# Performance work log

Hardware: AMD Instinct MI355X
Metric: run time of the kernel (lower is better)

The kernel has to match this reference:

```python
import jax, jax.numpy as jnp
import numpy as np

E, L, D, H, S, B = 8, 12, 768, 12, 512, 32
DIMS = [12, 8, 8, 8, 8, 12]
RANKS = [1, 8, 8, 8, 8, 8, 1]
ALPHA = 8.0


def setup_inputs() -> dict:
    key = jax.random.key(0)
    ks = iter(jax.random.split(key, 32))
    inp = {}
    inp['hidden_states'] = jax.random.normal(next(ks), (B, S, D), jnp.float32)
    inp['router_weights'] = jax.random.normal(next(ks), (D, E), jnp.float32)
    for pre in ('q', 'v'):
        for i in range(6):
            shp = (E, L, RANKS[i], DIMS[i], RANKS[i + 1])
            inp[f'{pre}_core{i}'] = jax.random.normal(next(ks), shp, jnp.float32) * 0.05
    for nm in ('Wq', 'Wk', 'Wv', 'Wo'):
        inp[nm] = jax.random.normal(next(ks), (L, D, D), jnp.float32) * 0.02
    for nm in ('bq', 'bk', 'bv', 'bo'):
        inp[nm] = jnp.zeros((L, D), jnp.float32)
    inp['ln_scale'] = jnp.ones((L, D), jnp.float32)
    inp['ln_bias'] = jnp.zeros((L, D), jnp.float32)
    return inp


def _layernorm(x, scale, bias, eps=1e-12):
    mu = x.mean(-1, keepdims=True)
    var = ((x - mu) ** 2).mean(-1, keepdims=True)
    return (x - mu) * jax.lax.rsqrt(var + eps) * scale + bias


def _tt_weights(cores):
    # cores[i]: [L, r_i, d_i, r_{i+1}]; chained TT contraction, vectorized over layers
    w = jnp.einsum('Lijk,Lklm,Lmno,Lopq,Lqrs,Lstu->Ljlnprt', *cores)
    return w.reshape(w.shape[0], D, D)  # [L, out, in] (matches torch weight.reshape)


def reference(hidden_states, router_weights,
              q_core0, q_core1, q_core2, q_core3, q_core4, q_core5,
              v_core0, v_core1, v_core2, v_core3, v_core4, v_core5,
              Wq, Wk, Wv, Wo, bq, bk, bv, bo, ln_scale, ln_bias):
    # routing: pool over sequence, softmax + argmax per sample
    pooled = hidden_states.mean(axis=1)                      # [B, D]
    probs = jax.nn.softmax(pooled @ router_weights, axis=-1)  # [B, E]
    idx = jnp.argmax(probs, axis=-1)                          # [B]
    e = idx[-1]
    qc = [c[e] for c in (q_core0, q_core1, q_core2, q_core3, q_core4, q_core5)]
    vc = [c[e] for c in (v_core0, v_core1, v_core2, v_core3, v_core4, v_core5)]
    Wq_a = Wq + ALPHA * _tt_weights(qc)  # [L, D, D]
    Wv_a = Wv + ALPHA * _tt_weights(vc)

    hd = D // H
    scale = 1.0 / jnp.sqrt(jnp.float32(hd))
    x = hidden_states
    for l in range(L):
        q = (x @ Wq_a[l].T + bq[l]).reshape(B, S, H, hd)
        k = (x @ Wk[l].T + bk[l]).reshape(B, S, H, hd)
        v = (x @ Wv_a[l].T + bv[l]).reshape(B, S, H, hd)
        scores = jnp.einsum('bqhd,bkhd->bhqk', q, k) * scale
        attn = jax.nn.softmax(scores, axis=-1)
        ctx = jnp.einsum('bhqk,bkhd->bqhd', attn, v).reshape(B, S, D)
        out = ctx @ Wo[l].T + bo[l]
        x = _layernorm(x + out, ln_scale[l], ln_bias[l])
    return x
```

## Files before the change

kernel.cpp:

```cpp
#include <hip/hip_runtime.h>
#include <hip/hip_bf16.h>
#include <stdint.h>

#define E_ 8
#define L_ 12
#define D_ 768
#define H_ 12
#define S_ 512
#define B_ 32
#define BS_ (B_*S_)

typedef __attribute__((ext_vector_type(4))) float floatx4;
typedef __attribute__((ext_vector_type(8))) __bf16 bf16x8;
typedef __attribute__((ext_vector_type(4))) __bf16 bf16x4;

__device__ __forceinline__ __bf16 f2bf(float f) {
  unsigned u = __builtin_bit_cast(unsigned, f);
  u += 0x7fffu + ((u >> 16) & 1u);
  unsigned short h = (unsigned short)(u >> 16);
  return __builtin_bit_cast(__bf16, h);
}

__device__ __forceinline__ float fexp2(float x) {
#if __has_builtin(__builtin_amdgcn_exp2f)
  return __builtin_amdgcn_exp2f(x);
#else
  return exp2f(x);
#endif
}

__device__ __forceinline__ void async16(const void* g, void* l) {
  __builtin_amdgcn_global_load_lds((__attribute__((address_space(1))) void*)g,
                                   (__attribute__((address_space(3))) void*)l,
                                   16, 0, 0);
}

__global__ void routing_pool_kernel(const float* __restrict__ hidden,
                                    float* __restrict__ partial) {
  const int blk = blockIdx.x;
  const int tid = threadIdx.x;
  const float* base = hidden + (size_t)(B_-1)*S_*D_ + (size_t)blk*8*D_;
  float acc[3] = {0.f, 0.f, 0.f};
  for (int s = 0; s < 8; ++s) {
#pragma unroll
    for (int i = 0; i < 3; ++i)
      acc[i] += base[(size_t)s*D_ + tid + i*256];
  }
#pragma unroll
  for (int i = 0; i < 3; ++i) partial[(size_t)blk*D_ + tid + i*256] = acc[i];
}

__global__ void routing_finish_kernel(const float* __restrict__ partial,
                                      const float* __restrict__ rw,
                                      int* __restrict__ e_out) {
  __shared__ float pooled[D_];
  __shared__ float logits[E_];
  int tid = threadIdx.x;
#pragma unroll
  for (int i = 0; i < 3; ++i) {
    int d = tid + i*256;
    float s = 0.f;
    for (int blk = 0; blk < 64; ++blk) s += partial[(size_t)blk*D_ + d];
    pooled[d] = s;
  }
  __syncthreads();
  if (tid < E_) {
    float s = 0.f;
    for (int d = 0; d < D_; ++d) s += pooled[d] * rw[d*E_ + tid];
    logits[tid] = s;
  }
  __syncthreads();
  if (tid == 0) {
    int best = 0; float bvv = logits[0];
    for (int e = 1; e < E_; ++e) if (logits[e] > bvv) { bvv = logits[e]; best = e; }
    e_out[0] = best;
  }
}

__global__ void convert_bf16_kernel(const float* __restrict__ src, __bf16* __restrict__ dst) {
  size_t i = ((size_t)blockIdx.x*256 + threadIdx.x)*8;
  __bf16 r[8];
#pragma unroll
  for (int j = 0; j < 8; ++j) r[j] = f2bf(src[i+j]);
  *(bf16x8*)(dst + i) = *(bf16x8*)r;
}

__global__ void convert_wk_kernel(const float* __restrict__ wk, __bf16* __restrict__ wqkv) {
  size_t i = ((size_t)blockIdx.x*256 + threadIdx.x)*8;
  int l = (int)(i / (D_*D_));
  int rem = (int)(i % (D_*D_));
  int n = rem / D_, k = rem % D_;
  __bf16 r[8];
#pragma unroll
  for (int j = 0; j < 8; ++j) r[j] = f2bf(wk[i+j]);
  *(bf16x8*)(wqkv + (size_t)l*2304*D_ + (size_t)(768+n)*D_ + k) = *(bf16x8*)r;
}

__global__ void tt_prep_kernel(
    const float* __restrict__ qc0, const float* __restrict__ qc1, const float* __restrict__ qc2,
    const float* __restrict__ qc3, const float* __restrict__ qc4, const float* __restrict__ qc5,
    const float* __restrict__ vc0, const float* __restrict__ vc1, const float* __restrict__ vc2,
    const float* __restrict__ vc3, const float* __restrict__ vc4, const float* __restrict__ vc5,
    const float* __restrict__ Wq, const float* __restrict__ Wv,
    const int* __restrict__ e_idx, __bf16* __restrict__ wqkv) {
  const int l = blockIdx.x;
  const int pre = blockIdx.y;
  const int z = blockIdx.z;
  const int tid = threadIdx.x;
  const int e = e_idx[0];
  const float* c0 = (pre ? vc0 : qc0) + (size_t)(e*L_ + l)*96;
  const float* c1 = (pre ? vc1 : qc1) + (size_t)(e*L_ + l)*512;
  const float* c2 = (pre ? vc2 : qc2) + (size_t)(e*L_ + l)*512;
  const float* c3 = (pre ? vc3 : qc3) + (size_t)(e*L_ + l)*512;
  const float* c4 = (pre ? vc4 : qc4) + (size_t)(e*L_ + l)*512;
  const float* c5 = (pre ? vc5 : qc5) + (size_t)(e*L_ + l)*96;
  __shared__ float M1[768];
  __shared__ float R2[768];
  __shared__ float M2[6144];
  __shared__ float Rm[6144];
  for (int idx = tid; idx < 768; idx += 256) {
    int j = idx >> 6, rem = idx & 63, l2 = rem >> 3, m = rem & 7;
    float s = 0.f;
    for (int k = 0; k < 8; ++k) s += c0[j*8 + k] * c1[k*64 + l2*8 + m];
    M1[idx] = s;
    int qq = idx / 96, rem2 = idx % 96, rr = rem2 / 12, t = rem2 % 12;
    float s2 = 0.f;
    for (int si = 0; si < 8; ++si) s2 += c4[qq*64 + rr*8 + si] * c5[si*12 + t];
    R2[idx] = s2;
  }
  __syncthreads();
  for (int idx = tid; idx < 6144; idx += 256) {
    int o = idx & 7, n = (idx >> 3) & 7, jl = idx >> 6;
    float s = 0.f;
    for (int m = 0; m < 8; ++m) s += M1[jl*8 + m] * c2[m*64 + n*8 + o];
    M2[idx] = s;
    int o2 = idx / 768, inp = idx % 768, p = inp / 96, rt = inp % 96;
    float s2 = 0.f;
    for (int qq = 0; qq < 8; ++qq) s2 += c3[o2*64 + p*8 + qq] * R2[qq*96 + rt];
    Rm[idx] = s2;
  }
  __syncthreads();
  const float* Wbase = (pre ? Wv : Wq) + (size_t)l*D_*D_;
  __bf16* dst = wqkv + (size_t)l*2304*D_ + (pre ? (size_t)1536*D_ : 0);
  for (int g = tid; g < 48*96; g += 256) {
    const int outr = z*48 + (g / 96);
    const int inp0 = (g % 96) * 8;
    float m2r[8];
#pragma unroll
    for (int o = 0; o < 8; ++o) m2r[o] = M2[outr*8 + o];
    float acc[8];
#pragma unroll
    for (int u = 0; u < 8; ++u) acc[u] = 0.f;
#pragma unroll
    for (int o = 0; o < 8; ++o) {
      float4 r0 = *(const float4*)&Rm[o*768 + inp0];
      float4 r1 = *(const float4*)&Rm[o*768 + inp0 + 4];
      acc[0] += m2r[o]*r0.x; acc[1] += m2r[o]*r0.y;
      acc[2] += m2r[o]*r0.z; acc[3] += m2r[o]*r0.w;
      acc[4] += m2r[o]*r1.x; acc[5] += m2r[o]*r1.y;
      acc[6] += m2r[o]*r1.z; acc[7] += m2r[o]*r1.w;
    }
    const float* wb = Wbase + (size_t)outr*768 + inp0;
    float4 w0 = *(const float4*)wb;
    float4 w1 = *(const float4*)(wb + 4);
    __bf16 r[8];
    r[0] = f2bf(w0.x + 8.f*acc[0]); r[1] = f2bf(w0.y + 8.f*acc[1]);
    r[2] = f2bf(w0.z + 8.f*acc[2]); r[3] = f2bf(w0.w + 8.f*acc[3]);
    r[4] = f2bf(w1.x + 8.f*acc[4]); r[5] = f2bf(w1.y + 8.f*acc[5]);
    r[6] = f2bf(w1.z + 8.f*acc[6]); r[7] = f2bf(w1.w + 8.f*acc[7]);
    *(bf16x8*)(dst + (size_t)outr*768 + inp0) = *(bf16x8*)r;
  }
}

#define SLOT_BYTES 28672
template<bool SPLITV>
__global__ __launch_bounds__(512, 2) void gemm_bt(
    const __bf16* __restrict__ A, const __bf16* __restrict__ Bw,
    const float* __restrict__ bq, const float* __restrict__ bk, const float* __restrict__ bvp,
    __bf16* __restrict__ outb, __bf16* __restrict__ vtout, int Nw) {
  __shared__ __align__(16) char lds[4*SLOT_BYTES];
  const int tid = threadIdx.x;
  const int w = tid >> 6, lane = tid & 63;
  const int quad = lane >> 4, l16 = lane & 15;
  const int wm = w >> 2, wn = w & 3;
  const size_t mblk = (size_t)blockIdx.y * 256;
  const size_t nblk = (size_t)blockIdx.x * 192;
  const __bf16* Ag = A + mblk * 768;
  const __bf16* Bg = Bw + nblk * 768;

  int a_goff[2], a_loff[2];
#pragma unroll
  for (int i = 0; i < 2; ++i) {
    int line = w*16 + i*8 + (lane >> 3);
    int s8 = (lane & 7) ^ (line & 7);
    int row = 2*line + (s8 >> 2);
    a_goff[i] = row*768 + (s8 & 3)*8;
    a_loff[i] = (w*16 + i*8)*128;
  }
  int b_goff[2], b_loff[2];
#pragma unroll
  for (int i = 0; i < 2; ++i) {
    int bl0 = (w < 4) ? (w*16 + i*8) : (64 + (w-4)*8);
    int line = bl0 + (lane >> 3);
    int s8 = (lane & 7) ^ (line & 7);
    int row = 2*line + (s8 >> 2);
    b_goff[i] = row*768 + (s8 & 3)*8;
    b_loff[i] = 16384 + bl0*128;
  }

  int a_foff[8], b_foff[3];
#pragma unroll
  for (int mf = 0; mf < 8; ++mf) {
    int r = wm*128 + mf*16 + l16;
    int line = r >> 1, s8 = (r & 1)*4 + quad, ph = s8 ^ (line & 7);
    a_foff[mf] = line*128 + ph*16;
  }
#pragma unroll
  for (int nf = 0; nf < 3; ++nf) {
    int r = wn*48 + nf*16 + l16;
    int line = r >> 1, s8 = (r & 1)*4 + quad, ph = s8 ^ (line & 7);
    b_foff[nf] = 16384 + line*128 + ph*16;
  }

  floatx4 acc[8][3];
#pragma unroll
  for (int mf = 0; mf < 8; ++mf)
#pragma unroll
    for (int nf = 0; nf < 3; ++nf) acc[mf][nf] = {0.f,0.f,0.f,0.f};

  auto STAGE = [&](int t) {
    const __bf16* Ab = Ag + t*32;
    const __bf16* Bb = Bg + t*32;
    char* ls = lds + (t & 3)*SLOT_BYTES;
    async16(Ab + a_goff[0], ls + a_loff[0]);
    async16(Ab + a_goff[1], ls + a_loff[1]);
    if (w < 4) {
      async16(Bb + b_goff[0], ls + b_loff[0]);
      async16(Bb + b_goff[1], ls + b_loff[1]);
    } else {
      async16(Bb + b_goff[0], ls + b_loff[0]);
    }
  };

  bf16x8 af[8], bfr[3];
  auto LOAD1 = [&](int u) {
    const char* ls = lds + (u & 3)*SLOT_BYTES;
#pragma unroll
    for (int nf = 0; nf < 3; ++nf) bfr[nf] = *(const bf16x8*)(ls + b_foff[nf]);
#pragma unroll
    for (int mf = 0; mf < 4; ++mf) af[mf] = *(const bf16x8*)(ls + a_foff[mf]);
  };
  auto LOAD2 = [&](int u) {
    const char* ls = lds + (u & 3)*SLOT_BYTES;
#pragma unroll
    for (int mf = 4; mf < 8; ++mf) af[mf] = *(const bf16x8*)(ls + a_foff[mf]);
  };
  auto MM = [&](int mf0) {
    __builtin_amdgcn_s_setprio(1);
#pragma unroll
    for (int mf = mf0; mf < mf0 + 4; ++mf)
#pragma unroll
      for (int nf = 0; nf < 3; ++nf)
        acc[mf][nf] = __builtin_amdgcn_mfma_f32_16x16x32_bf16(af[mf], bfr[nf], acc[mf][nf], 0, 0, 0);
    __builtin_amdgcn_s_setprio(0);
  };
  auto BAR = [&]() {
    __builtin_amdgcn_s_barrier();
    __builtin_amdgcn_sched_barrier(0);
  };

  STAGE(0); STAGE(1); STAGE(2);
  if (w < 4) asm volatile("s_waitcnt vmcnt(8)" ::: "memory");
  else       asm volatile("s_waitcnt vmcnt(6)" ::: "memory");
  BAR();

  for (int u = 0; u < 21; ++u) {
    LOAD1(u);
    BAR();
    MM(0);
    LOAD2(u);
    STAGE(u + 3);
    if (w < 4) asm volatile("s_waitcnt vmcnt(8)" ::: "memory");
    else       asm volatile("s_waitcnt vmcnt(6)" ::: "memory");
    BAR();
    MM(4);
  }
  LOAD1(21);
  BAR();
  MM(0);
  LOAD2(21);
  if (w < 4) asm volatile("s_waitcnt vmcnt(4)" ::: "memory");
  else       asm volatile("s_waitcnt vmcnt(3)" ::: "memory");
  BAR();
  MM(4);
  LOAD1(22);
  BAR();
  MM(0);
  LOAD2(22);
  asm volatile("s_waitcnt vmcnt(0)" ::: "memory");
  BAR();
  MM(4);
  LOAD1(23);
  BAR();
  MM(0);
  LOAD2(23);
  BAR();
  MM(4);

  if (SPLITV && blockIdx.x >= 8) {
#pragma unroll
    for (int nf = 0; nf < 3; ++nf) {
      const int vcol = (int)nblk - 1536 + wn*48 + nf*16 + l16;
      const int h = vcol >> 6, d = vcol & 63;
      const float bval = bvp[vcol];
#pragma unroll
      for (int mf = 0; mf < 8; ++mf) {
        const int mrow = (int)mblk + wm*128 + mf*16 + quad*4;
        const int b = mrow >> 9, s = mrow & 511;
        __bf16 pr[4];
#pragma unroll
        for (int r = 0; r < 4; ++r) pr[r] = f2bf(acc[mf][nf][r] + bval);
        *(bf16x4*)(vtout + (size_t)((b*H_ + h)*64 + d)*S_ + s) = *(bf16x4*)pr;
      }
    }
    return;
  }
  const float* bias = bq;
  if (SPLITV) bias = (blockIdx.x < 4) ? bq : bk;
  float bval[3]; int ncol[3];
#pragma unroll
  for (int nf = 0; nf < 3; ++nf) {
    ncol[nf] = (int)nblk + wn*48 + nf*16 + l16;
    int bc = ncol[nf]; if (bc >= 768) bc -= 768;
    bval[nf] = bias[bc];
  }
#pragma unroll
  for (int mf = 0; mf < 8; ++mf) {
#pragma unroll
    for (int nf = 0; nf < 3; ++nf) {
#pragma unroll
      for (int r = 0; r < 4; ++r) {
        const int mrow = (int)mblk + wm*128 + mf*16 + quad*4 + r;
        outb[(size_t)mrow*Nw + ncol[nf]] = f2bf(acc[mf][nf][r] + bval[nf]);
      }
    }
  }
}

#define PSTR 72
__global__ __launch_bounds__(256) void flash_kernel(const __bf16* __restrict__ qkv,
                                                    const __bf16* __restrict__ vt,
                                                    __bf16* __restrict__ ctx) {
  __shared__ __align__(16) __bf16 Qs[64*PSTR];
  __shared__ __align__(16) __bf16 Ks[64*PSTR];
  __shared__ __align__(16) __bf16 Vts[64*PSTR];
  __shared__ __align__(16) __bf16 Ps[64*PSTR];
  const int tid = threadIdx.x;
  const int w = tid >> 6, lane = tid & 63;
  const int quad = lane >> 4, l16 = lane & 15;
  const int n = blockIdx.x;
  const int bh = (n >> 6)*8 + (n & 7);
  const int q0 = ((n >> 3) & 7) * 64;
  const int b = bh / H_, h = bh % H_;
  const float SCL = 0.125f * 1.44269504f;

  {
#pragma unroll
    for (int it = 0; it < 2; ++it) {
      int slot = it*256 + tid, row = slot >> 3, seg = slot & 7;
      bf16x8 v = *(const bf16x8*)(qkv + (size_t)(b*S_ + q0 + row)*2304 + h*64 + seg*8);
      *(bf16x8*)&Qs[row*PSTR + seg*8] = v;
    }
  }

  floatx4 acc_o[4];
#pragma unroll
  for (int jd = 0; jd < 4; ++jd) acc_o[jd] = {0.f,0.f,0.f,0.f};
  float m_prev = -__builtin_inff();
  float l_part = 0.f;

  for (int kt = 0; kt < 8; ++kt) {
    __syncthreads();
#pragma unroll
    for (int it = 0; it < 2; ++it) {
      int slot = it*256 + tid, row = slot >> 3, seg = slot & 7;
      bf16x8 kvv = *(const bf16x8*)(qkv + (size_t)(b*S_ + kt*64 + row)*2304 + 768 + h*64 + seg*8);
      bf16x8 vtv = *(const bf16x8*)(vt + (size_t)(bh*64 + row)*S_ + kt*64 + seg*8);
      *(bf16x8*)&Ks[row*PSTR + seg*8] = kvv;
      *(bf16x8*)&Vts[row*PSTR + seg*8] = vtv;
    }
    __syncthreads();
    floatx4 sacc[4];
#pragma unroll
    for (int i = 0; i < 4; ++i) sacc[i] = {0.f,0.f,0.f,0.f};
#pragma unroll
    for (int kk = 0; kk < 64; kk += 32) {
      bf16x8 bq_ = *(const bf16x8*)&Qs[(w*16 + l16)*PSTR + kk + quad*8];
#pragma unroll
      for (int i = 0; i < 4; ++i) {
        bf16x8 ak = *(const bf16x8*)&Ks[(i*16 + l16)*PSTR + kk + quad*8];
        sacc[i] = __builtin_amdgcn_mfma_f32_16x16x32_bf16(ak, bq_, sacc[i], 0, 0, 0);
      }
    }
    float sv[4][4];
#pragma unroll
    for (int i = 0; i < 4; ++i)
#pragma unroll
      for (int r = 0; r < 4; ++r) sv[i][r] = sacc[i][r] * SCL;
    float mloc = sv[0][0];
#pragma unroll
    for (int i = 0; i < 4; ++i)
#pragma unroll
      for (int r = 0; r < 4; ++r) mloc = fmaxf(mloc, sv[i][r]);
    mloc = fmaxf(mloc, __shfl_xor(mloc, 16));
    mloc = fmaxf(mloc, __shfl_xor(mloc, 32));
    float mnew = fmaxf(m_prev, mloc);
    float alpha = fexp2(m_prev - mnew);
    m_prev = mnew;
    float rsum = 0.f;
#pragma unroll
    for (int i = 0; i < 4; ++i) {
      __bf16 pr[4];
#pragma unroll
      for (int r = 0; r < 4; ++r) {
        float p = fexp2(sv[i][r] - mnew);
        rsum += p;
        pr[r] = f2bf(p);
      }
      *(bf16x4*)&Ps[(w*16 + l16)*PSTR + i*16 + quad*4] = *(bf16x4*)pr;
    }
    l_part = l_part*alpha + rsum;
    float ab[4];
#pragma unroll
    for (int r = 0; r < 4; ++r) ab[r] = __shfl(alpha, quad*4 + r);
#pragma unroll
    for (int jd = 0; jd < 4; ++jd)
#pragma unroll
      for (int r = 0; r < 4; ++r) acc_o[jd][r] *= ab[r];
#pragma unroll
    for (int kk = 0; kk < 64; kk += 32) {
      bf16x8 ap = *(const bf16x8*)&Ps[(w*16 + l16)*PSTR + kk + quad*8];
#pragma unroll
      for (int jd = 0; jd < 4; ++jd) {
        bf16x8 bv_ = *(const bf16x8*)&Vts[(jd*16 + l16)*PSTR + kk + quad*8];
        acc_o[jd] = __builtin_amdgcn_mfma_f32_16x16x32_bf16(ap, bv_, acc_o[jd], 0, 0, 0);
      }
    }
  }
  float l_tot = l_part;
  l_tot += __shfl_xor(l_tot, 16);
  l_tot += __shfl_xor(l_tot, 32);
  float lb[4];
#pragma unroll
  for (int r = 0; r < 4; ++r) lb[r] = __shfl(l_tot, quad*4 + r);
#pragma unroll
  for (int jd = 0; jd < 4; ++jd) {
    const int d = jd*16 + l16;
#pragma unroll
    for (int r = 0; r < 4; ++r) {
      const int q = q0 + w*16 + quad*4 + r;
      ctx[(size_t)(b*S_ + q)*D_ + h*64 + d] = f2bf(acc_o[jd][r] / lb[r]);
    }
  }
}

template<bool FIRST, bool LAST>
__global__ __launch_bounds__(256) void ln_kernel(const float* __restrict__ residf,
                                                 __bf16* xb,
                                                 const __bf16* __restrict__ proj,
                                                 const float* __restrict__ gamma,
                                                 const float* __restrict__ beta,
                                                 float* __restrict__ xoutf) {
  const int tid = threadIdx.x;
  const int w = tid >> 6, lane = tid & 63;
  const int row = blockIdx.x*4 + w;
  const size_t base = (size_t)row * D_;
  const int c0 = lane*8;
  const bool has2 = lane < 32;
  const int c1 = 512 + lane*8;

  float v0[8], v1[8];
  {
    bf16x8 p0 = *(const bf16x8*)(proj + base + c0);
    if (FIRST) {
      float4 a = *(const float4*)(residf + base + c0);
      float4 bq4 = *(const float4*)(residf + base + c0 + 4);
      v0[0]=a.x+(float)p0[0]; v0[1]=a.y+(float)p0[1]; v0[2]=a.z+(float)p0[2]; v0[3]=a.w+(float)p0[3];
      v0[4]=bq4.x+(float)p0[4]; v0[5]=bq4.y+(float)p0[5]; v0[6]=bq4.z+(float)p0[6]; v0[7]=bq4.w+(float)p0[7];
    } else {
      bf16x8 r0 = *(const bf16x8*)(xb + base + c0);
#pragma unroll
      for (int j = 0; j < 8; ++j) v0[j] = (float)r0[j] + (float)p0[j];
    }
    if (has2) {
      bf16x8 p1 = *(const bf16x8*)(proj + base + c1);
      if (FIRST) {
        float4 a = *(const float4*)(residf + base + c1);
        float4 bq4 = *(const float4*)(residf + base + c1 + 4);
        v1[0]=a.x+(float)p1[0]; v1[1]=a.y+(float)p1[1]; v1[2]=a.z+(float)p1[2]; v1[3]=a.w+(float)p1[3];
        v1[4]=bq4.x+(float)p1[4]; v1[5]=bq4.y+(float)p1[5]; v1[6]=bq4.z+(float)p1[6]; v1[7]=bq4.w+(float)p1[7];
      } else {
        bf16x8 r1 = *(const bf16x8*)(xb + base + c1);
#pragma unroll
        for (int j = 0; j < 8; ++j) v1[j] = (float)r1[j] + (float)p1[j];
      }
    } else {
#pragma unroll
      for (int j = 0; j < 8; ++j) v1[j] = 0.f;
    }
  }
  float s = 0.f;
#pragma unroll
  for (int j = 0; j < 8; ++j) s += v0[j] + v1[j];
#pragma unroll
  for (int off = 32; off; off >>= 1) s += __shfl_xor(s, off);
  const float mu = s * (1.f/768.f);
  float q = 0.f;
#pragma unroll
  for (int j = 0; j < 8; ++j) { float d0 = v0[j]-mu; q += d0*d0; }
  if (has2) {
#pragma unroll
    for (int j = 0; j < 8; ++j) { float d1 = v1[j]-mu; q += d1*d1; }
  }
#pragma unroll
  for (int off = 32; off; off >>= 1) q += __shfl_xor(q, off);
  const float rs = rsqrtf(q * (1.f/768.f) + 1e-12f);

  {
    float4 g0 = *(const float4*)(gamma + c0);
    float4 g1 = *(const float4*)(gamma + c0 + 4);
    float4 b0 = *(const float4*)(beta + c0);
    float4 b1 = *(const float4*)(beta + c0 + 4);
    float o[8];
    o[0]=(v0[0]-mu)*rs*g0.x+b0.x; o[1]=(v0[1]-mu)*rs*g0.y+b0.y;
    o[2]=(v0[2]-mu)*rs*g0.z+b0.z; o[3]=(v0[3]-mu)*rs*g0.w+b0.w;
    o[4]=(v0[4]-mu)*rs*g1.x+b1.x; o[5]=(v0[5]-mu)*rs*g1.y+b1.y;
    o[6]=(v0[6]-mu)*rs*g1.z+b1.z; o[7]=(v0[7]-mu)*rs*g1.w+b1.w;
    if (LAST) {
      *(float4*)(xoutf + base + c0)     = {o[0],o[1],o[2],o[3]};
      *(float4*)(xoutf + base + c0 + 4) = {o[4],o[5],o[6],o[7]};
    } else {
      __bf16 ob[8];
#pragma unroll
      for (int j = 0; j < 8; ++j) ob[j] = f2bf(o[j]);
      *(bf16x8*)(xb + base + c0) = *(bf16x8*)ob;
    }
  }
  if (has2) {
    float4 g0 = *(const float4*)(gamma + c1);
    float4 g1 = *(const float4*)(gamma + c1 + 4);
    float4 b0 = *(const float4*)(beta + c1);
    float4 b1 = *(const float4*)(beta + c1 + 4);
    float o[8];
    o[0]=(v1[0]-mu)*rs*g0.x+b0.x; o[1]=(v1[1]-mu)*rs*g0.y+b0.y;
    o[2]=(v1[2]-mu)*rs*g0.z+b0.z; o[3]=(v1[3]-mu)*rs*g0.w+b0.w;
    o[4]=(v1[4]-mu)*rs*g1.x+b1.x; o[5]=(v1[5]-mu)*rs*g1.y+b1.y;
    o[6]=(v1[6]-mu)*rs*g1.z+b1.z; o[7]=(v1[7]-mu)*rs*g1.w+b1.w;
    if (LAST) {
      *(float4*)(xoutf + base + c1)     = {o[0],o[1],o[2],o[3]};
      *(float4*)(xoutf + base + c1 + 4) = {o[4],o[5],o[6],o[7]};
    } else {
      __bf16 ob[8];
#pragma unroll
      for (int j = 0; j < 8; ++j) ob[j] = f2bf(o[j]);
      *(bf16x8*)(xb + base + c1) = *(bf16x8*)ob;
    }
  }
}

extern "C" void kernel_launch(void* const* d_in, const int* in_sizes, int n_in,
                              void* d_out, int out_size, void* d_ws, size_t ws_size,
                              hipStream_t stream) {
  const float* hidden = (const float*)d_in[0];
  const float* router = (const float*)d_in[1];
  const float* qc[6]; const float* vc[6];
  for (int i = 0; i < 6; ++i) qc[i] = (const float*)d_in[2+i];
  for (int i = 0; i < 6; ++i) vc[i] = (const float*)d_in[8+i];
  const float* Wq = (const float*)d_in[14];
  const float* Wk = (const float*)d_in[15];
  const float* Wv = (const float*)d_in[16];
  const float* Wo = (const float*)d_in[17];
  const float* bq = (const float*)d_in[18];
  const float* bk = (const float*)d_in[19];
  const float* bv = (const float*)d_in[20];
  const float* bo = (const float*)d_in[21];
  const float* lns = (const float*)d_in[22];
  const float* lnb = (const float*)d_in[23];
  float* out = (float*)d_out;

  char* ws = (char*)d_ws;
  size_t off = 0;
  auto alloc = [&](size_t bytes) -> void* {
    off = (off + 255) & ~(size_t)255;
    void* p = ws + off; off += bytes; return p;
  };
  int*    e_idx = (int*)   alloc(4);
  float*  rpart = (float*) alloc((size_t)64*D_*4);
  __bf16* xbf   = (__bf16*)alloc((size_t)BS_*D_*2);
  __bf16* qkv   = (__bf16*)alloc((size_t)BS_*2304*2);
  __bf16* vt    = (__bf16*)alloc((size_t)B_*H_*64*S_*2);
  __bf16* ctx   = (__bf16*)alloc((size_t)BS_*D_*2);
  __bf16* projb = (__bf16*)alloc((size_t)BS_*D_*2);
  __bf16* wqkv  = (__bf16*)alloc((size_t)L_*2304*D_*2);
  __bf16* wobf  = (__bf16*)alloc((size_t)L_*D_*D_*2);
  (void)ws_size; (void)in_sizes; (void)n_in; (void)out_size;

  routing_pool_kernel<<<64, 256, 0, stream>>>(hidden, rpart);
  routing_finish_kernel<<<1, 256, 0, stream>>>(rpart, router, e_idx);
  convert_bf16_kernel<<<(BS_*D_)/2048, 256, 0, stream>>>(hidden, xbf);
  tt_prep_kernel<<<dim3(L_, 2, 16), 256, 0, stream>>>(qc[0],qc[1],qc[2],qc[3],qc[4],qc[5],
                                                      vc[0],vc[1],vc[2],vc[3],vc[4],vc[5],
                                                      Wq, Wv, e_idx, wqkv);
  convert_wk_kernel<<<(L_*D_*D_)/2048, 256, 0, stream>>>(Wk, wqkv);
  convert_bf16_kernel<<<(L_*D_*D_)/2048, 256, 0, stream>>>(Wo, wobf);

  for (int l = 0; l < L_; ++l) {
    gemm_bt<true><<<dim3(12,64), 512, 0, stream>>>(xbf, wqkv + (size_t)l*2304*D_,
        bq + l*D_, bk + l*D_, bv + l*D_, qkv, vt, 2304);
    flash_kernel<<<3072, 256, 0, stream>>>(qkv, vt, ctx);
    gemm_bt<false><<<dim3(4,64), 512, 0, stream>>>(ctx, wobf + (size_t)l*D_*D_,
        bo + l*D_, nullptr, nullptr, projb, nullptr, 768);
    if (l == 0)
      ln_kernel<true,false><<<BS_/4, 256, 0, stream>>>(hidden, xbf, projb,
          lns + l*D_, lnb + l*D_, nullptr);
    else if (l == L_-1)
      ln_kernel<false,true><<<BS_/4, 256, 0, stream>>>(nullptr, xbf, projb,
          lns + l*D_, lnb + l*D_, out);
    else
      ln_kernel<false,false><<<BS_/4, 256, 0, stream>>>(nullptr, xbf, projb,
          lns + l*D_, lnb + l*D_, nullptr);
  }
}
```

Baseline: 2.470 ms.

## Register-prefetch next K/V tile in flash attention and raise MFMA wave priority

The flash attention kernel now loads the next K and V^T tile from global memory into registers while it computes on the current tile. This hides global load latency behind the MFMA and softmax work, using ping-pong register buffers with the loop unrolled by two. The barriers become raw s_barrier calls with explicit lgkmcnt waits and sched_barrier fences. s_setprio is raised around the MFMA blocks. In exchange the kernel uses more VGPRs, which may lower occupancy.

```diff
diff --git a/kernel.cpp b/kernel.cpp
--- a/kernel.cpp
+++ b/kernel.cpp
@@ -364,13 +364,20 @@
   const int b = bh / H_, h = bh % H_;
   const float SCL = 0.125f * 1.44269504f;
 
+  const int row0 = tid >> 3,        seg0 = tid & 7;
+  const int row1 = (256 + tid) >> 3, seg1 = tid & 7;
+
+  bf16x8 ka[2], va[2], kb[2], vb[2];
+  ka[0] = *(const bf16x8*)(qkv + (size_t)(b*S_ + row0)*2304 + 768 + h*64 + seg0*8);
+  va[0] = *(const bf16x8*)(vt  + (size_t)(bh*64 + row0)*S_ + seg0*8);
+  ka[1] = *(const bf16x8*)(qkv + (size_t)(b*S_ + row1)*2304 + 768 + h*64 + seg1*8);
+  va[1] = *(const bf16x8*)(vt  + (size_t)(bh*64 + row1)*S_ + seg1*8);
+
   {
-#pragma unroll
-    for (int it = 0; it < 2; ++it) {
-      int slot = it*256 + tid, row = slot >> 3, seg = slot & 7;
-      bf16x8 v = *(const bf16x8*)(qkv + (size_t)(b*S_ + q0 + row)*2304 + h*64 + seg*8);
-      *(bf16x8*)&Qs[row*PSTR + seg*8] = v;
-    }
+    bf16x8 v0 = *(const bf16x8*)(qkv + (size_t)(b*S_ + q0 + row0)*2304 + h*64 + seg0*8);
+    bf16x8 v1 = *(const bf16x8*)(qkv + (size_t)(b*S_ + q0 + row1)*2304 + h*64 + seg1*8);
+    *(bf16x8*)&Qs[row0*PSTR + seg0*8] = v0;
+    *(bf16x8*)&Qs[row1*PSTR + seg1*8] = v1;
   }
 
   floatx4 acc_o[4];
@@ -379,20 +386,28 @@
   float m_prev = -__builtin_inff();
   float l_part = 0.f;
 
-  for (int kt = 0; kt < 8; ++kt) {
-    __syncthreads();
-#pragma unroll
-    for (int it = 0; it < 2; ++it) {
-      int slot = it*256 + tid, row = slot >> 3, seg = slot & 7;
-      bf16x8 kvv = *(const bf16x8*)(qkv + (size_t)(b*S_ + kt*64 + row)*2304 + 768 + h*64 + seg*8);
-      bf16x8 vtv = *(const bf16x8*)(vt + (size_t)(bh*64 + row)*S_ + kt*64 + seg*8);
-      *(bf16x8*)&Ks[row*PSTR + seg*8] = kvv;
-      *(bf16x8*)&Vts[row*PSTR + seg*8] = vtv;
-    }
-    __syncthreads();
+  auto STEP = [&](int kt, bf16x8* ck, bf16x8* cv, bf16x8* nk, bf16x8* nv, bool pf) {
+    asm volatile("s_waitcnt lgkmcnt(0)" ::: "memory");
+    __builtin_amdgcn_s_barrier();
+    __builtin_amdgcn_sched_barrier(0);
+    *(bf16x8*)&Ks[row0*PSTR + seg0*8]  = ck[0];
+    *(bf16x8*)&Vts[row0*PSTR + seg0*8] = cv[0];
+    *(bf16x8*)&Ks[row1*PSTR + seg1*8]  = ck[1];
+    *(bf16x8*)&Vts[row1*PSTR + seg1*8] = cv[1];
+    if (pf) {
+      nk[0] = *(const bf16x8*)(qkv + (size_t)(b*S_ + (kt+1)*64 + row0)*2304 + 768 + h*64 + seg0*8);
+      nv[0] = *(const bf16x8*)(vt  + (size_t)(bh*64 + row0)*S_ + (kt+1)*64 + seg0*8);
+      nk[1] = *(const bf16x8*)(qkv + (size_t)(b*S_ + (kt+1)*64 + row1)*2304 + 768 + h*64 + seg1*8);
+      nv[1] = *(const bf16x8*)(vt  + (size_t)(bh*64 + row1)*S_ + (kt+1)*64 + seg1*8);
+    }
+    asm volatile("s_waitcnt lgkmcnt(0)" ::: "memory");
+    __builtin_amdgcn_s_barrier();
+    __builtin_amdgcn_sched_barrier(0);
+
     floatx4 sacc[4];
 #pragma unroll
     for (int i = 0; i < 4; ++i) sacc[i] = {0.f,0.f,0.f,0.f};
+    __builtin_amdgcn_s_setprio(1);
 #pragma unroll
     for (int kk = 0; kk < 64; kk += 32) {
       bf16x8 bq_ = *(const bf16x8*)&Qs[(w*16 + l16)*PSTR + kk + quad*8];
@@ -402,16 +417,16 @@
         sacc[i] = __builtin_amdgcn_mfma_f32_16x16x32_bf16(ak, bq_, sacc[i], 0, 0, 0);
       }
     }
-    float sv[4][4];
+    __builtin_amdgcn_s_setprio(0);
 #pragma unroll
     for (int i = 0; i < 4; ++i)
 #pragma unroll
-      for (int r = 0; r < 4; ++r) sv[i][r] = sacc[i][r] * SCL;
-    float mloc = sv[0][0];
+      for (int r = 0; r < 4; ++r) sacc[i][r] *= SCL;
+    float mloc = sacc[0][0];
 #pragma unroll
     for (int i = 0; i < 4; ++i)
 #pragma unroll
-      for (int r = 0; r < 4; ++r) mloc = fmaxf(mloc, sv[i][r]);
+      for (int r = 0; r < 4; ++r) mloc = fmaxf(mloc, sacc[i][r]);
     mloc = fmaxf(mloc, __shfl_xor(mloc, 16));
     mloc = fmaxf(mloc, __shfl_xor(mloc, 32));
     float mnew = fmaxf(m_prev, mloc);
@@ -423,7 +438,7 @@
       __bf16 pr[4];
 #pragma unroll
       for (int r = 0; r < 4; ++r) {
-        float p = fexp2(sv[i][r] - mnew);
+        float p = fexp2(sacc[i][r] - mnew);
         rsum += p;
         pr[r] = f2bf(p);
       }
@@ -440,13 +455,22 @@
 #pragma unroll
     for (int kk = 0; kk < 64; kk += 32) {
       bf16x8 ap = *(const bf16x8*)&Ps[(w*16 + l16)*PSTR + kk + quad*8];
+      __builtin_amdgcn_s_setprio(1);
 #pragma unroll
       for (int jd = 0; jd < 4; ++jd) {
         bf16x8 bv_ = *(const bf16x8*)&Vts[(jd*16 + l16)*PSTR + kk + quad*8];
         acc_o[jd] = __builtin_amdgcn_mfma_f32_16x16x32_bf16(ap, bv_, acc_o[jd], 0, 0, 0);
       }
-    }
-  }
+      __builtin_amdgcn_s_setprio(0);
+    }
+  };
+
+#pragma unroll
+  for (int kt2 = 0; kt2 < 8; kt2 += 2) {
+    STEP(kt2,     ka, va, kb, vb, true);
+    STEP(kt2 + 1, kb, vb, ka, va, kt2 + 1 < 7);
+  }
+
   float l_tot = l_part;
   l_tot += __shfl_xor(l_tot, 16);
   l_tot += __shfl_xor(l_tot, 32);
```

Result: no change. 2.446 ms (-1.0%).
